# Kernel optimization log

Hardware: AMD Instinct MI355X
Metric: run time of the kernel (lower is better)

The kernel has to match this reference:

```python
import jax, jax.numpy as jnp
import numpy as np
import math

NX = 1024
N_HEAD = 16
HEAD_DIM = NX // N_HEAD
N_CTX = 2048
REL_VOCAB = 64
B = 2
S = 2048


def setup_inputs() -> dict:
    key = jax.random.key(0)
    ks = jax.random.split(key, 7)
    x = jax.random.normal(ks[0], (B, S, NX), dtype=jnp.float32)
    rel = jax.random.randint(ks[1], (B, S, S), 0, REL_VOCAB, dtype=jnp.int64)
    sc = 0.02
    Wqkv = jax.random.normal(ks[2], (NX, 3 * NX), dtype=jnp.float32) * sc
    bqkv = jnp.zeros((3 * NX,), dtype=jnp.float32)
    Wproj = jax.random.normal(ks[3], (NX, NX), dtype=jnp.float32) * sc
    bproj = jnp.zeros((NX,), dtype=jnp.float32)
    rel_emb = jax.random.normal(ks[4], (REL_VOCAB, N_HEAD), dtype=jnp.float32) * sc
    return {"x": x, "Wqkv": Wqkv, "bqkv": bqkv, "Wproj": Wproj,
            "bproj": bproj, "rel_emb": rel_emb, "rel": rel}


def reference(x, Wqkv, bqkv, Wproj, bproj, rel_emb, rel):
    Bsz, Sq, _ = x.shape
    qkv = x @ Wqkv + bqkv                      # [B,S,3*nx]
    q, k, v = jnp.split(qkv, 3, axis=-1)
    def split_heads(t):                        # [B,S,nx] -> [B,H,S,D]
        return t.reshape(Bsz, Sq, N_HEAD, HEAD_DIM).transpose(0, 2, 1, 3)
    q, k, v = split_heads(q), split_heads(k), split_heads(v)
    w = jnp.einsum('bhqd,bhkd->bhqk', q, k) / math.sqrt(HEAD_DIM)
    bmask = jnp.tril(jnp.ones((Sq, Sq), dtype=w.dtype))[None, None]  # [1,1,S,S]
    w = w * bmask - 1e10 * (1.0 - bmask)
    relw = rel_emb[rel].transpose(0, 3, 1, 2)  # [B,S,S,H] -> [B,H,S,S]
    w = w * (relw * bmask)                     # faithful: masked scores become 0
    p = jax.nn.softmax(w, axis=-1)
    a = jnp.einsum('bhqk,bhkd->bhqd', p, v)
    a = a.transpose(0, 2, 1, 3).reshape(Bsz, Sq, NX)  # merge heads
    return a @ Wproj + bproj
```

## Files before the change

### kernel.cpp

```cpp
#include <hip/hip_runtime.h>

typedef unsigned short u16;
typedef unsigned char u8;
typedef __attribute__((ext_vector_type(8))) short short8;
typedef __attribute__((ext_vector_type(4))) short short4v;
typedef __attribute__((ext_vector_type(4))) float f32x4;

#define GLD16(g, l) __builtin_amdgcn_global_load_lds( \
    (const __attribute__((address_space(1))) void*)(g), \
    (__attribute__((address_space(3))) void*)(l), 16, 0, 0)

__device__ __forceinline__ float bf2f(u16 u){
  union { unsigned int i; float f; } v; v.i = ((unsigned int)u) << 16; return v.f;
}
__device__ __forceinline__ u16 f2bf(float f){
  union { float f; unsigned int i; } v; v.f = f;
  unsigned int u = v.i;
  unsigned int r = (u + 0x7FFFu + ((u >> 16) & 1u)) >> 16;
  return (u16)r;
}

__device__ __forceinline__ f32x4 mfma16(short4v a, short4v b, f32x4 c){
#if __has_builtin(__builtin_amdgcn_mfma_f32_16x16x16bf16_1k)
  return __builtin_amdgcn_mfma_f32_16x16x16bf16_1k(a, b, c, 0, 0, 0);
#else
  asm volatile("s_nop 1\n\tv_mfma_f32_16x16x16_bf16 %0, %1, %2, %0" : "+v"(c) : "v"(a), "v"(b));
  return c;
#endif
}

__global__ __launch_bounds__(256) void prep_k(const float* __restrict__ x, u16* __restrict__ xb,
                                              const float* __restrict__ Wqkv, u16* __restrict__ wqkvT,
                                              const float* __restrict__ Wproj, u16* __restrict__ wprojT,
                                              const int* __restrict__ rel, u8* __restrict__ rel8){
  const int bid = blockIdx.x, t = threadIdx.x;
  if (bid < 4096){
    int i = bid * 256 + t;
    float4 v = ((const float4*)x)[i];
    unsigned long long pk = (unsigned long long)f2bf(v.x)
      | ((unsigned long long)f2bf(v.y) << 16)
      | ((unsigned long long)f2bf(v.z) << 32)
      | ((unsigned long long)f2bf(v.w) << 48);
    ((unsigned long long*)xb)[i] = pk;
  } else if (bid < 8192){
    const float* W; u16* Wt; int K, N, blk, nbx;
    if (bid < 7168){ W = Wqkv; Wt = wqkvT; K = 1024; N = 3072; blk = bid - 4096; nbx = 96; }
    else           { W = Wproj; Wt = wprojT; K = 1024; N = 1024; blk = bid - 7168; nbx = 32; }
    __shared__ float tl[32][33];
    int n0 = (blk % nbx) * 32, k0 = (blk / nbx) * 32;
    int tx = t & 31, ty = t >> 5;
    for (int i = ty; i < 32; i += 8)
      tl[i][tx] = W[(size_t)(k0 + i) * N + n0 + tx];
    __syncthreads();
    for (int i = ty; i < 32; i += 8)
      Wt[(size_t)(n0 + i) * K + k0 + tx] = f2bf(tl[tx][i]);
  } else {
    int i = (bid - 8192) * 256 + t;
    int4 v = ((const int4*)rel)[i];
    unsigned int pk = (unsigned int)(v.x & 255) | ((unsigned int)(v.y & 255) << 8)
      | ((unsigned int)(v.z & 255) << 16) | ((unsigned int)(v.w & 255) << 24);
    ((unsigned int*)rel8)[i] = pk;
  }
}

__global__ __launch_bounds__(256) void gemm_qkv_k(const u16* __restrict__ A, const u16* __restrict__ Bt,
                                                  const float* __restrict__ bias,
                                                  u16* __restrict__ oq, u16* __restrict__ okk, u16* __restrict__ vt){
  __shared__ u16 la[3][128 * 32];
  __shared__ u16 lb[3][128 * 32];
  const int K = 1024;
  const int t = threadIdx.x, w = t >> 6, lane = t & 63;
  const int l15 = lane & 15, l4 = lane >> 4;
  const int m0 = blockIdx.y * 128, n0 = blockIdx.x * 128;
  const int wr = w >> 1, wc = w & 1;
  f32x4 acc[4][4] = {};
  const u16* Abase = A + (size_t)m0 * K;
  const u16* Bbase = Bt + (size_t)n0 * K;

  const int srow0 = t >> 2, srow1 = 64 + (t >> 2);
  const int cg = t & 3;
  const int sc0 = cg ^ (srow0 & 3), sc1 = cg ^ (srow1 & 3);
  const int wbase0 = (w * 64) * 8, wbase1 = (256 + w * 64) * 8;

#define QSTAGE(kt, buf) do {                                                        \
    GLD16(Abase + (size_t)srow0 * K + (kt) * 32 + sc0 * 8, &la[buf][wbase0]);       \
    GLD16(Abase + (size_t)srow1 * K + (kt) * 32 + sc1 * 8, &la[buf][wbase1]);       \
    GLD16(Bbase + (size_t)srow0 * K + (kt) * 32 + sc0 * 8, &lb[buf][wbase0]);       \
    GLD16(Bbase + (size_t)srow1 * K + (kt) * 32 + sc1 * 8, &lb[buf][wbase1]);       \
  } while (0)

  QSTAGE(0, 0);
  QSTAGE(1, 1);
  for (int ki = 0; ki < 32; ++ki){
    __builtin_amdgcn_sched_barrier(0);
    if (ki < 31) asm volatile("s_waitcnt vmcnt(4)" ::: "memory");
    else         asm volatile("s_waitcnt vmcnt(0)" ::: "memory");
    __builtin_amdgcn_s_barrier();
    __builtin_amdgcn_sched_barrier(0);
    if (ki + 2 < 32) QSTAGE(ki + 2, (ki + 2) % 3);
    const int cb = ki % 3;
    short8 af[4], bfr[4];
#pragma unroll
    for (int mi = 0; mi < 4; ++mi){
      int row = wr * 64 + mi * 16 + l15;
      af[mi] = *(const short8*)&la[cb][row * 32 + ((l4 ^ (row & 3)) * 8)];
    }
#pragma unroll
    for (int ni = 0; ni < 4; ++ni){
      int row = wc * 64 + ni * 16 + l15;
      bfr[ni] = *(const short8*)&lb[cb][row * 32 + ((l4 ^ (row & 3)) * 8)];
    }
    __builtin_amdgcn_s_setprio(1);
#pragma unroll
    for (int mi = 0; mi < 4; ++mi)
#pragma unroll
      for (int ni = 0; ni < 4; ++ni)
        acc[mi][ni] = __builtin_amdgcn_mfma_f32_16x16x32_bf16(af[mi], bfr[ni], acc[mi][ni], 0, 0, 0);
    __builtin_amdgcn_s_setprio(0);
  }
#undef QSTAGE

#pragma unroll
  for (int mi = 0; mi < 4; ++mi){
    const int m_base = m0 + wr * 64 + mi * 16 + l4 * 4;
    const int bsel = m_base >> 11, s0q = m_base & 2047;
#pragma unroll
    for (int ni = 0; ni < 4; ++ni){
      int n = n0 + wc * 64 + ni * 16 + l15;
      float vb = bias[n];
      int tt = n >> 10, rr = n & 1023, head = rr >> 6, dd = rr & 63;
      if (tt == 2){
        int c = s0q >> 6, w6 = s0q & 63;
        int pj0 = (((w6 >> 2) & 3) << 4) | (((w6 >> 4) & 3) << 2);
        u16 o4[4];
#pragma unroll
        for (int r = 0; r < 4; ++r) o4[r] = f2bf(acc[mi][ni][r] + vb);
        *(uint2*)(vt + ((size_t)(bsel * 16 + head) * 64 + dd) * 2048 + c * 64 + pj0) = *(const uint2*)o4;
      } else {
        u16* dst = (tt == 0) ? oq : okk;
#pragma unroll
        for (int r = 0; r < 4; ++r)
          dst[(((size_t)(bsel * 16 + head)) * 2048 + s0q + r) * 64 + dd] = f2bf(acc[mi][ni][r] + vb);
      }
    }
  }
}

template<int BN>
__global__ __launch_bounds__(256) void gemm_bt_k(const u16* __restrict__ A, const u16* __restrict__ Bt,
                                                 const float* __restrict__ bias, float* __restrict__ of,
                                                 int M, int N, int K){
  __shared__ u16 la[128 * 64];
  __shared__ u16 lb[BN * 64];
  const int t = threadIdx.x, w = t >> 6, lane = t & 63;
  const int l15 = lane & 15, l4 = lane >> 4;
  const int m0 = blockIdx.y * 128, n0 = blockIdx.x * BN;
  const int wr = w >> 1, wc = w & 1;
  constexpr int NI = BN / 32;
  f32x4 acc[4][NI] = {};
  const u16* Abase = A + (size_t)m0 * K;
  const u16* Bbase = Bt + (size_t)n0 * K;
  for (int kt = 0; kt < K; kt += 64){
    __syncthreads();
#pragma unroll
    for (int i = 0; i < 4; ++i){
      int chunk = i * 256 + t;
      int row = chunk >> 3, cs = chunk & 7;
      int c = cs ^ (row & 7);
      GLD16(Abase + (size_t)row * K + kt + c * 8, &la[(i * 256 + w * 64) * 8]);
    }
#pragma unroll
    for (int i = 0; i < BN / 32; ++i){
      int chunk = i * 256 + t;
      int row = chunk >> 3, cs = chunk & 7;
      int c = cs ^ (row & 7);
      GLD16(Bbase + (size_t)row * K + kt + c * 8, &lb[(i * 256 + w * 64) * 8]);
    }
    asm volatile("s_waitcnt vmcnt(0)" ::: "memory");
    __syncthreads();
    short8 af[4][2], bfr[NI][2];
#pragma unroll
    for (int mi = 0; mi < 4; ++mi){
      int row = wr * 64 + mi * 16 + l15;
#pragma unroll
      for (int h = 0; h < 2; ++h)
        af[mi][h] = *(const short8*)&la[row * 64 + (((h * 4 + l4) ^ (row & 7)) * 8)];
    }
#pragma unroll
    for (int ni = 0; ni < NI; ++ni){
      int row = wc * (BN / 2) + ni * 16 + l15;
#pragma unroll
      for (int h = 0; h < 2; ++h)
        bfr[ni][h] = *(const short8*)&lb[row * 64 + (((h * 4 + l4) ^ (row & 7)) * 8)];
    }
#pragma unroll
    for (int mi = 0; mi < 4; ++mi)
#pragma unroll
      for (int ni = 0; ni < NI; ++ni){
        acc[mi][ni] = __builtin_amdgcn_mfma_f32_16x16x32_bf16(af[mi][0], bfr[ni][0], acc[mi][ni], 0, 0, 0);
        acc[mi][ni] = __builtin_amdgcn_mfma_f32_16x16x32_bf16(af[mi][1], bfr[ni][1], acc[mi][ni], 0, 0, 0);
      }
  }
#pragma unroll
  for (int mi = 0; mi < 4; ++mi){
#pragma unroll
    for (int ni = 0; ni < NI; ++ni){
#pragma unroll
      for (int r = 0; r < 4; ++r){
        int m = m0 + wr * 64 + mi * 16 + l4 * 4 + r;
        int n = n0 + wc * (BN / 2) + ni * 16 + l15;
        of[(size_t)m * N + n] = acc[mi][ni][r] + bias[n];
      }
    }
  }
}

__global__ __launch_bounds__(256) void vsuf2_k(const u16* __restrict__ vt, float* __restrict__ vsuf){
  __shared__ float part[32][64];
  const int bh = blockIdx.x;
  const int d = threadIdx.x & 63, qtr = threadIdx.x >> 6;
  const u16* row = vt + ((size_t)bh * 64 + d) * 2048;
  for (int c = qtr * 8; c < qtr * 8 + 8; ++c){
    float s = 0.f;
#pragma unroll
    for (int jv = 0; jv < 8; ++jv){
      short8 v = *(const short8*)(row + c * 64 + jv * 8);
#pragma unroll
      for (int e = 0; e < 8; ++e) s += bf2f((u16)v[e]);
    }
    part[c][d] = s;
  }
  __syncthreads();
  if (threadIdx.x < 64){
    float run = 0.f;
    vsuf[((size_t)bh * 33 + 32) * 64 + d] = 0.f;
    for (int c = 31; c >= 0; --c){
      run += part[c][d];
      vsuf[((size_t)bh * 33 + c) * 64 + d] = run;
    }
  }
}

template<int U8, int SPLIT>
__global__ __launch_bounds__(256, 4) void attn_k(const u16* __restrict__ qb, const u16* __restrict__ kb,
                                                 const u16* __restrict__ vt, const float* __restrict__ vsuf,
                                                 const void* __restrict__ relp, const float* __restrict__ rel_emb,
                                                 u16* __restrict__ ab, float* __restrict__ pacc,
                                                 float* __restrict__ prsum){
  __shared__ u16 Kt[2][64 * 64];
  __shared__ u16 Vt[2][64 * 64];
  __shared__ float remb[64];
  int p, hf, bh;
  if (SPLIT){
    const int lid = blockIdx.x;
    const int bhgrp = lid & 7, within = (lid >> 3) & 3, pf = lid >> 5;
    bh = bhgrp * 4 + within;
    p = pf >> 1; hf = pf & 1;
  } else {
    p = blockIdx.x; hf = 0; bh = blockIdx.y;
  }
  const int b = bh >> 4, h = bh & 15;
  const int TA = p, TB = 31 - p;
  const int q0A = TA * 64, q0B = TB * 64;
  const int tid = threadIdx.x, w = tid >> 6, lane = tid & 63;
  const int l15 = lane & 15, l4 = lane >> 4;
  if (tid < 64) remb[tid] = rel_emb[tid * 16 + h] * (0.125f * 1.44269504088896f);
  const u16* kbh = kb + ((size_t)bh * 2048) * 64;
  const u16* vbh = vt + ((size_t)bh * 64) * 2048;
  const u16* qA = qb + (((size_t)bh * 2048) + q0A + w * 16 + l15) * 64 + l4 * 8;
  const u16* qB = qb + (((size_t)bh * 2048) + q0B + w * 16 + l15) * 64 + l4 * 8;
  const short8 aqA0 = *(const short8*)qA, aqA1 = *(const short8*)(qA + 32);
  const short8 aqB0 = *(const short8*)qB, aqB1 = *(const short8*)(qB + 32);
  const u8*  r8A  = (const u8*)relp + ((size_t)b * 2048 + q0A + w * 16 + l15) * 2048;
  const u8*  r8B  = (const u8*)relp + ((size_t)b * 2048 + q0B + w * 16 + l15) * 2048;
  const int* r32A = (const int*)relp + ((size_t)b * 2048 + q0A + w * 16 + l15) * 2048;
  const int* r32B = (const int*)relp + ((size_t)b * 2048 + q0B + w * 16 + l15) * 2048;

  const int srow0 = (tid >> 3), srow1 = 32 + (tid >> 3);
  const int scs = tid & 7;
  const int sc0 = scs ^ (srow0 & 7), sc1 = scs ^ (srow1 & 7);
  const int sldsoff = (w * 64) * 8;

#define STAGE(ktile, buf) do {                                                       \
    GLD16(kbh + (size_t)((ktile) * 64 + srow0) * 64 + sc0 * 8, &Kt[buf][sldsoff]);   \
    GLD16(kbh + (size_t)((ktile) * 64 + srow1) * 64 + sc1 * 8, &Kt[buf][2048 + sldsoff]); \
    GLD16(vbh + (size_t)srow0 * 2048 + (ktile) * 64 + sc0 * 8, &Vt[buf][sldsoff]);   \
    GLD16(vbh + (size_t)srow1 * 2048 + (ktile) * 64 + sc1 * 8, &Vt[buf][2048 + sldsoff]); \
  } while (0)

  f32x4 acc[4] = {};
  float rsum = 0.f;
  unsigned int relc[4], reln[4];

  auto relload = [&](bool isA, int kt, unsigned int* dst){
    int off = kt * 64 + 4 * l4;
    if (U8){
      const u8* pp = isA ? r8A : r8B;
#pragma unroll
      for (int t = 0; t < 4; ++t) dst[t] = *(const unsigned int*)(pp + off + 16 * t);
    } else {
      const int* pp = isA ? r32A : r32B;
#pragma unroll
      for (int t = 0; t < 4; ++t){
        int4 v4 = *(const int4*)(pp + off + 16 * t);
        dst[t] = (unsigned int)(v4.x & 255) | ((unsigned int)(v4.y & 255) << 8)
               | ((unsigned int)(v4.z & 255) << 16) | ((unsigned int)(v4.w & 255) << 24);
      }
    }
  };

  auto writeout = [&](int Td, int q0){
    asm volatile("s_nop 7\n\ts_nop 7" :::);
    float s = rsum;
    s += __shfl_xor(s, 16);
    s += __shfl_xor(s, 32);
    float invZ = 1.f / (s + (float)(2048 - (Td + 1) * 64));
    int qg = q0 + w * 16 + l15;
    const float* sufp = vsuf + ((size_t)bh * 33 + Td + 1) * 64;
#pragma unroll
    for (int ni = 0; ni < 4; ++ni){
      float4 sv = *(const float4*)(sufp + ni * 16 + 4 * l4);
      unsigned int lo2 = (unsigned int)f2bf((acc[ni][0] + sv.x) * invZ)
                       | ((unsigned int)f2bf((acc[ni][1] + sv.y) * invZ) << 16);
      unsigned int hi2 = (unsigned int)f2bf((acc[ni][2] + sv.z) * invZ)
                       | ((unsigned int)f2bf((acc[ni][3] + sv.w) * invZ) << 16);
      uint2 o; o.x = lo2; o.y = hi2;
      *(uint2*)(ab + ((size_t)b * 2048 + qg) * 1024 + h * 64 + ni * 16 + 4 * l4) = o;
    }
  };

  const int lo = (SPLIT && hf) ? 17 : 0;
  const int hi = (SPLIT && !hf) ? 17 : 33;

  {
    bool isA0 = (lo <= TA);
    int kt0 = isA0 ? lo : lo - TA - 1;
    STAGE(kt0, 0);
    relload(isA0, kt0, relc);
  }
  __syncthreads();

  for (int it = lo; it < hi; ++it){
    const bool isA = (it <= TA);
    const int kt = isA ? it : (it - TA - 1);
    const int cur = (it - lo) & 1;

    if (it + 1 < hi){
      const bool nA = (it + 1 <= TA);
      const int nkt = nA ? (it + 1) : (it - TA);
      STAGE(nkt, cur ^ 1);
      relload(nA, nkt, reln);
    }

    const short8 a0 = isA ? aqA0 : aqB0;
    const short8 a1 = isA ? aqA1 : aqB1;
    const bool diag = (kt == (isA ? TA : TB));

    short4v pk[4];
    __builtin_amdgcn_s_setprio(1);
#pragma unroll
    for (int t = 0; t < 4; ++t){
      const int krow = 16 * t + l15;
      const u16* kbase = &Kt[cur][krow * 64];
      short8 bk0 = *(const short8*)&kbase[((l4)     ^ (krow & 7)) * 8];
      short8 bk1 = *(const short8*)&kbase[((4 + l4) ^ (krow & 7)) * 8];
      f32x4 sf = {0.f, 0.f, 0.f, 0.f};
      sf = __builtin_amdgcn_mfma_f32_16x16x32_bf16(bk0, a0, sf, 0, 0, 0);
      sf = __builtin_amdgcn_mfma_f32_16x16x32_bf16(bk1, a1, sf, 0, 0, 0);
      unsigned int rw = relc[t];
      const int kk = 16 * t + 4 * l4;
      float prv[4];
#pragma unroll
      for (int r = 0; r < 4; ++r){
        float sc = sf[r] * remb[(rw >> (8 * r)) & 255];
        if (diag) sc = (kk + r <= w * 16 + l15) ? sc : 0.f;
        float pv = __builtin_amdgcn_exp2f(sc);
        rsum += pv;
        prv[r] = pv;
      }
      union { unsigned int u[2]; short4v s; } pu;
      asm("v_cvt_pk_bf16_f32 %0, %1, %2" : "=v"(pu.u[0]) : "v"(prv[0]), "v"(prv[1]));
      asm("v_cvt_pk_bf16_f32 %0, %1, %2" : "=v"(pu.u[1]) : "v"(prv[2]), "v"(prv[3]));
      pk[t] = pu.s;
    }
    asm volatile("s_nop 2" :::);
#pragma unroll
    for (int ni = 0; ni < 4; ++ni){
      const int drow = ni * 16 + l15;
      const u16* vbase = &Vt[cur][drow * 64];
      short8 vv0 = *(const short8*)&vbase[(((2 * l4)     ^ (drow & 7))) * 8];
      short8 vv1 = *(const short8*)&vbase[(((2 * l4 + 1) ^ (drow & 7))) * 8];
      short4v va0 = {vv0[0], vv0[1], vv0[2], vv0[3]};
      short4v va1 = {vv0[4], vv0[5], vv0[6], vv0[7]};
      short4v va2 = {vv1[0], vv1[1], vv1[2], vv1[3]};
      short4v va3 = {vv1[4], vv1[5], vv1[6], vv1[7]};
      acc[ni] = mfma16(va0, pk[0], acc[ni]);
      acc[ni] = mfma16(va1, pk[1], acc[ni]);
      acc[ni] = mfma16(va2, pk[2], acc[ni]);
      acc[ni] = mfma16(va3, pk[3], acc[ni]);
    }
    __builtin_amdgcn_s_setprio(0);

    if (it == TA){
      writeout(TA, q0A);
#pragma unroll
      for (int ni = 0; ni < 4; ++ni) acc[ni] = f32x4{0.f, 0.f, 0.f, 0.f};
      rsum = 0.f;
    }
    if (it + 1 < hi){
#pragma unroll
      for (int t = 0; t < 4; ++t) relc[t] = reln[t];
    }
    __syncthreads();
  }
#undef STAGE

  if (SPLIT){
    asm volatile("s_nop 7\n\ts_nop 7" :::);
    float s = rsum;
    s += __shfl_xor(s, 16);
    s += __shfl_xor(s, 32);
    const size_t slot = (((size_t)bh * 16 + p) * 2 + hf);
    float* pslot = pacc + slot * 4096;
#pragma unroll
    for (int ni = 0; ni < 4; ++ni)
      *(f32x4*)(pslot + (w * 16 + l15) * 64 + ni * 16 + 4 * l4) = acc[ni];
    if (l4 == 0) prsum[slot * 64 + w * 16 + l15] = s;
  } else {
    writeout(TB, q0B);
  }
}

__global__ __launch_bounds__(256) void attn_fin_k(const float* __restrict__ pacc,
                                                  const float* __restrict__ prsum,
                                                  const float* __restrict__ vsuf,
                                                  u16* __restrict__ ab){
  const int p = blockIdx.x, bh = blockIdx.y;
  const int b = bh >> 4, h = bh & 15;
  const int TB = 31 - p, q0 = TB * 64;
  const int r = threadIdx.x >> 2, cg = threadIdx.x & 3;
  const size_t slot = ((size_t)bh * 16 + p) * 2;
  const size_t base = slot * 4096 + r * 64 + cg * 16;
  float rs = prsum[slot * 64 + r] + prsum[(slot + 1) * 64 + r];
  float invZ = 1.f / (rs + (float)(2048 - (TB + 1) * 64));
  const float* sufp = vsuf + ((size_t)bh * 33 + TB + 1) * 64 + cg * 16;
  u16 o[16];
#pragma unroll
  for (int j = 0; j < 4; ++j){
    f32x4 a0 = *(const f32x4*)(pacc + base + j * 4);
    f32x4 a1 = *(const f32x4*)(pacc + base + 4096 + j * 4);
    f32x4 sv = *(const f32x4*)(sufp + j * 4);
#pragma unroll
    for (int e = 0; e < 4; ++e) o[j * 4 + e] = f2bf((a0[e] + a1[e] + sv[e]) * invZ);
  }
  u16* dst = ab + ((size_t)b * 2048 + q0 + r) * 1024 + h * 64 + cg * 16;
  *(uint4*)dst = *(const uint4*)&o[0];
  *(uint4*)(dst + 8) = *(const uint4*)&o[8];
}

extern "C" void kernel_launch(void* const* d_in, const int* in_sizes, int n_in,
                              void* d_out, int out_size, void* d_ws, size_t ws_size,
                              hipStream_t stream){
  const float* x       = (const float*)d_in[0];
  const float* Wqkv    = (const float*)d_in[1];
  const float* bqkv    = (const float*)d_in[2];
  const float* Wproj   = (const float*)d_in[3];
  const float* bproj   = (const float*)d_in[4];
  const float* rel_emb = (const float*)d_in[5];
  const int*   rel     = (const int*)d_in[6];
  float* out = (float*)d_out;

  char* ws = (char*)d_ws;
  u16* xb     = (u16*)(ws);
  u16* wqkvT  = (u16*)(ws + (8ull  << 20));
  u16* wprojT = (u16*)(ws + (14ull << 20));
  u16* qb     = (u16*)(ws + (16ull << 20));
  u16* kb     = (u16*)(ws + (24ull << 20));
  u16* vtb    = (u16*)(ws + (40ull << 20));
  float* vsuf = (float*)(ws + (48ull << 20));
  float* pacc = (float*)(ws + (49ull << 20));
  float* prsum= (float*)(ws + (65ull << 20) + (512ull << 10));
  u8*   rel8  = (u8*)(ws + (66ull << 20));
  const bool useSplit = ws_size >= (67ull << 20);
  const bool useU8    = ws_size >= (75ull << 20);

  prep_k<<<useU8 ? 16384 : 8192, 256, 0, stream>>>(x, xb, Wqkv, wqkvT, Wproj, wprojT, rel, rel8);
  gemm_qkv_k<<<dim3(24, 32), 256, 0, stream>>>(xb, wqkvT, bqkv, qb, kb, vtb);
  vsuf2_k<<<32, 256, 0, stream>>>(vtb, vsuf);
  if (useU8)
    attn_k<1, 1><<<dim3(1024), 256, 0, stream>>>(qb, kb, vtb, vsuf, rel8, rel_emb, xb, pacc, prsum);
  else if (useSplit)
    attn_k<0, 1><<<dim3(1024), 256, 0, stream>>>(qb, kb, vtb, vsuf, rel, rel_emb, xb, pacc, prsum);
  else
    attn_k<0, 0><<<dim3(16, 32), 256, 0, stream>>>(qb, kb, vtb, vsuf, rel, rel_emb, xb, pacc, prsum);
  if (useSplit || useU8)
    attn_fin_k<<<dim3(16, 32), 256, 0, stream>>>(pacc, prsum, vsuf, xb);
  gemm_bt_k<64><<<dim3(16, 32), 256, 0, stream>>>(xb, wprojT, bproj, out, 4096, 1024, 1024);
}
```

Measured before the change: 138.9 us.

## Triple-buffer projection GEMM loads and replace LDS rel-emb lookup with bpermute

```diff
diff --git a/kernel.cpp b/kernel.cpp
--- a/kernel.cpp
+++ b/kernel.cpp
@@ -146,69 +146,69 @@
   }
 }
 
-template<int BN>
-__global__ __launch_bounds__(256) void gemm_bt_k(const u16* __restrict__ A, const u16* __restrict__ Bt,
-                                                 const float* __restrict__ bias, float* __restrict__ of,
-                                                 int M, int N, int K){
-  __shared__ u16 la[128 * 64];
-  __shared__ u16 lb[BN * 64];
+__global__ __launch_bounds__(256) void gemm_proj_k(const u16* __restrict__ A, const u16* __restrict__ Bt,
+                                                   const float* __restrict__ bias, float* __restrict__ of){
+  __shared__ u16 la[3][128 * 32];
+  __shared__ u16 lb[3][64 * 32];
+  const int K = 1024, N = 1024;
   const int t = threadIdx.x, w = t >> 6, lane = t & 63;
   const int l15 = lane & 15, l4 = lane >> 4;
-  const int m0 = blockIdx.y * 128, n0 = blockIdx.x * BN;
+  const int m0 = blockIdx.y * 128, n0 = blockIdx.x * 64;
   const int wr = w >> 1, wc = w & 1;
-  constexpr int NI = BN / 32;
-  f32x4 acc[4][NI] = {};
+  f32x4 acc[4][2] = {};
   const u16* Abase = A + (size_t)m0 * K;
   const u16* Bbase = Bt + (size_t)n0 * K;
-  for (int kt = 0; kt < K; kt += 64){
-    __syncthreads();
-#pragma unroll
-    for (int i = 0; i < 4; ++i){
-      int chunk = i * 256 + t;
-      int row = chunk >> 3, cs = chunk & 7;
-      int c = cs ^ (row & 7);
-      GLD16(Abase + (size_t)row * K + kt + c * 8, &la[(i * 256 + w * 64) * 8]);
-    }
-#pragma unroll
-    for (int i = 0; i < BN / 32; ++i){
-      int chunk = i * 256 + t;
-      int row = chunk >> 3, cs = chunk & 7;
-      int c = cs ^ (row & 7);
-      GLD16(Bbase + (size_t)row * K + kt + c * 8, &lb[(i * 256 + w * 64) * 8]);
-    }
-    asm volatile("s_waitcnt vmcnt(0)" ::: "memory");
-    __syncthreads();
-    short8 af[4][2], bfr[NI][2];
+
+  const int srow0 = t >> 2, srow1 = 64 + (t >> 2);
+  const int cg = t & 3;
+  const int sc0 = cg ^ (srow0 & 3), sc1 = cg ^ (srow1 & 3);
+  const int wbase0 = (w * 64) * 8, wbase1 = (256 + w * 64) * 8;
+
+#define PSTAGE(kt, buf) do {                                                        \
+    GLD16(Abase + (size_t)srow0 * K + (kt) * 32 + sc0 * 8, &la[buf][wbase0]);       \
+    GLD16(Abase + (size_t)srow1 * K + (kt) * 32 + sc1 * 8, &la[buf][wbase1]);       \
+    GLD16(Bbase + (size_t)srow0 * K + (kt) * 32 + sc0 * 8, &lb[buf][wbase0]);       \
+  } while (0)
+
+  PSTAGE(0, 0);
+  PSTAGE(1, 1);
+  for (int ki = 0; ki < 32; ++ki){
+    __builtin_amdgcn_sched_barrier(0);
+    if (ki < 31) asm volatile("s_waitcnt vmcnt(3)" ::: "memory");
+    else         asm volatile("s_waitcnt vmcnt(0)" ::: "memory");
+    __builtin_amdgcn_s_barrier();
+    __builtin_amdgcn_sched_barrier(0);
+    if (ki + 2 < 32) PSTAGE(ki + 2, (ki + 2) % 3);
+    const int cb = ki % 3;
+    short8 af[4], bfr[2];
 #pragma unroll
     for (int mi = 0; mi < 4; ++mi){
       int row = wr * 64 + mi * 16 + l15;
-#pragma unroll
-      for (int h = 0; h < 2; ++h)
-        af[mi][h] = *(const short8*)&la[row * 64 + (((h * 4 + l4) ^ (row & 7)) * 8)];
-    }
-#pragma unroll
-    for (int ni = 0; ni < NI; ++ni){
-      int row = wc * (BN / 2) + ni * 16 + l15;
-#pragma unroll
-      for (int h = 0; h < 2; ++h)
-        bfr[ni][h] = *(const short8*)&lb[row * 64 + (((h * 4 + l4) ^ (row & 7)) * 8)];
-    }
+      af[mi] = *(const short8*)&la[cb][row * 32 + ((l4 ^ (row & 3)) * 8)];
+    }
+#pragma unroll
+    for (int ni = 0; ni < 2; ++ni){
+      int row = wc * 32 + ni * 16 + l15;
+      bfr[ni] = *(const short8*)&lb[cb][row * 32 + ((l4 ^ (row & 3)) * 8)];
+    }
+    __builtin_amdgcn_s_setprio(1);
 #pragma unroll
     for (int mi = 0; mi < 4; ++mi)
 #pragma unroll
-      for (int ni = 0; ni < NI; ++ni){
-        acc[mi][ni] = __builtin_amdgcn_mfma_f32_16x16x32_bf16(af[mi][0], bfr[ni][0], acc[mi][ni], 0, 0, 0);
-        acc[mi][ni] = __builtin_amdgcn_mfma_f32_16x16x32_bf16(af[mi][1], bfr[ni][1], acc[mi][ni], 0, 0, 0);
-      }
-  }
+      for (int ni = 0; ni < 2; ++ni)
+        acc[mi][ni] = __builtin_amdgcn_mfma_f32_16x16x32_bf16(af[mi], bfr[ni], acc[mi][ni], 0, 0, 0);
+    __builtin_amdgcn_s_setprio(0);
+  }
+#undef PSTAGE
+
 #pragma unroll
   for (int mi = 0; mi < 4; ++mi){
 #pragma unroll
-    for (int ni = 0; ni < NI; ++ni){
+    for (int ni = 0; ni < 2; ++ni){
 #pragma unroll
       for (int r = 0; r < 4; ++r){
         int m = m0 + wr * 64 + mi * 16 + l4 * 4 + r;
-        int n = n0 + wc * (BN / 2) + ni * 16 + l15;
+        int n = n0 + wc * 32 + ni * 16 + l15;
         of[(size_t)m * N + n] = acc[mi][ni][r] + bias[n];
       }
     }
@@ -249,7 +249,6 @@
                                                  float* __restrict__ prsum){
   __shared__ u16 Kt[2][64 * 64];
   __shared__ u16 Vt[2][64 * 64];
-  __shared__ float remb[64];
   int p, hf, bh;
   if (SPLIT){
     const int lid = blockIdx.x;
@@ -264,7 +263,7 @@
   const int q0A = TA * 64, q0B = TB * 64;
   const int tid = threadIdx.x, w = tid >> 6, lane = tid & 63;
   const int l15 = lane & 15, l4 = lane >> 4;
-  if (tid < 64) remb[tid] = rel_emb[tid * 16 + h] * (0.125f * 1.44269504088896f);
+  const int remb_bits = __float_as_int(rel_emb[lane * 16 + h] * (0.125f * 1.44269504088896f));
   const u16* kbh = kb + ((size_t)bh * 2048) * 64;
   const u16* vbh = vt + ((size_t)bh * 64) * 2048;
   const u16* qA = qb + (((size_t)bh * 2048) + q0A + w * 16 + l15) * 64 + l4 * 8;
@@ -372,7 +371,9 @@
       float prv[4];
 #pragma unroll
       for (int r = 0; r < 4; ++r){
-        float sc = sf[r] * remb[(rw >> (8 * r)) & 255];
+        int idx4 = (int)((rw >> (8 * r)) & 255u) << 2;
+        float rwf = __int_as_float(__builtin_amdgcn_ds_bpermute(idx4, remb_bits));
+        float sc = sf[r] * rwf;
         if (diag) sc = (kk + r <= w * 16 + l15) ? sc : 0.f;
         float pv = __builtin_amdgcn_exp2f(sc);
         rsum += pv;
@@ -495,5 +496,5 @@
     attn_k<0, 0><<<dim3(16, 32), 256, 0, stream>>>(qb, kb, vtb, vsuf, rel, rel_emb, xb, pacc, prsum);
   if (useSplit || useU8)
     attn_fin_k<<<dim3(16, 32), 256, 0, stream>>>(pacc, prsum, vsuf, xb);
-  gemm_bt_k<64><<<dim3(16, 32), 256, 0, stream>>>(xb, wprojT, bproj, out, 4096, 1024, 1024);
-}
+  gemm_proj_k<<<dim3(16, 32), 256, 0, stream>>>(xb, wprojT, bproj, out);
+}
```

After: 142.0 us. 2.3% more time.

## Split attention key range into three chunks with bf16 partials and bpermute lookup

Applied to the files above, without the earlier changes.

```diff
diff --git a/kernel.cpp b/kernel.cpp
--- a/kernel.cpp
+++ b/kernel.cpp
@@ -245,26 +245,25 @@
 __global__ __launch_bounds__(256, 4) void attn_k(const u16* __restrict__ qb, const u16* __restrict__ kb,
                                                  const u16* __restrict__ vt, const float* __restrict__ vsuf,
                                                  const void* __restrict__ relp, const float* __restrict__ rel_emb,
-                                                 u16* __restrict__ ab, float* __restrict__ pacc,
+                                                 u16* __restrict__ ab, u16* __restrict__ paccb,
                                                  float* __restrict__ prsum){
   __shared__ u16 Kt[2][64 * 64];
   __shared__ u16 Vt[2][64 * 64];
-  __shared__ float remb[64];
-  int p, hf, bh;
+  int p, u_, bh;
   if (SPLIT){
     const int lid = blockIdx.x;
-    const int bhgrp = lid & 7, within = (lid >> 3) & 3, pf = lid >> 5;
+    const int bhgrp = lid & 7, within = (lid >> 3) & 3, pu = lid >> 5;
     bh = bhgrp * 4 + within;
-    p = pf >> 1; hf = pf & 1;
+    p = pu / 3; u_ = pu % 3;
   } else {
-    p = blockIdx.x; hf = 0; bh = blockIdx.y;
+    p = blockIdx.x; u_ = 0; bh = blockIdx.y;
   }
   const int b = bh >> 4, h = bh & 15;
   const int TA = p, TB = 31 - p;
   const int q0A = TA * 64, q0B = TB * 64;
   const int tid = threadIdx.x, w = tid >> 6, lane = tid & 63;
   const int l15 = lane & 15, l4 = lane >> 4;
-  if (tid < 64) remb[tid] = rel_emb[tid * 16 + h] * (0.125f * 1.44269504088896f);
+  const int remb_bits = __float_as_int(rel_emb[lane * 16 + h] * (0.125f * 1.44269504088896f));
   const u16* kbh = kb + ((size_t)bh * 2048) * 64;
   const u16* vbh = vt + ((size_t)bh * 64) * 2048;
   const u16* qA = qb + (((size_t)bh * 2048) + q0A + w * 16 + l15) * 64 + l4 * 8;
@@ -329,8 +328,26 @@
     }
   };
 
-  const int lo = (SPLIT && hf) ? 17 : 0;
-  const int hi = (SPLIT && !hf) ? 17 : 33;
+  auto emitP = [&](int t01){
+    asm volatile("s_nop 7\n\ts_nop 7" :::);
+    float s = rsum;
+    s += __shfl_xor(s, 16);
+    s += __shfl_xor(s, 32);
+    const size_t slot = (((size_t)bh * 16 + p) * 3 + u_) * 2 + t01;
+    u16* pbase = paccb + slot * 4096 + (size_t)(w * 16 + l15) * 64;
+#pragma unroll
+    for (int ni = 0; ni < 4; ++ni){
+      unsigned int w0, w1;
+      asm("v_cvt_pk_bf16_f32 %0, %1, %2" : "=v"(w0) : "v"(acc[ni][0]), "v"(acc[ni][1]));
+      asm("v_cvt_pk_bf16_f32 %0, %1, %2" : "=v"(w1) : "v"(acc[ni][2]), "v"(acc[ni][3]));
+      uint2 o; o.x = w0; o.y = w1;
+      *(uint2*)(pbase + ni * 16 + 4 * l4) = o;
+    }
+    if (l4 == 0) prsum[slot * 64 + w * 16 + l15] = s;
+  };
+
+  const int lo = SPLIT ? 11 * u_ : 0;
+  const int hi = SPLIT ? lo + 11 : 33;
 
   {
     bool isA0 = (lo <= TA);
@@ -372,16 +389,18 @@
       float prv[4];
 #pragma unroll
       for (int r = 0; r < 4; ++r){
-        float sc = sf[r] * remb[(rw >> (8 * r)) & 255];
+        int idx4 = (int)((rw >> (8 * r)) & 255u) << 2;
+        float rwf = __int_as_float(__builtin_amdgcn_ds_bpermute(idx4, remb_bits));
+        float sc = sf[r] * rwf;
         if (diag) sc = (kk + r <= w * 16 + l15) ? sc : 0.f;
         float pv = __builtin_amdgcn_exp2f(sc);
         rsum += pv;
         prv[r] = pv;
       }
-      union { unsigned int u[2]; short4v s; } pu;
-      asm("v_cvt_pk_bf16_f32 %0, %1, %2" : "=v"(pu.u[0]) : "v"(prv[0]), "v"(prv[1]));
-      asm("v_cvt_pk_bf16_f32 %0, %1, %2" : "=v"(pu.u[1]) : "v"(prv[2]), "v"(prv[3]));
-      pk[t] = pu.s;
+      union { unsigned int u[2]; short4v s; } pu2;
+      asm("v_cvt_pk_bf16_f32 %0, %1, %2" : "=v"(pu2.u[0]) : "v"(prv[0]), "v"(prv[1]));
+      asm("v_cvt_pk_bf16_f32 %0, %1, %2" : "=v"(pu2.u[1]) : "v"(prv[2]), "v"(prv[3]));
+      pk[t] = pu2.s;
     }
     asm volatile("s_nop 2" :::);
 #pragma unroll
@@ -402,7 +421,8 @@
     __builtin_amdgcn_s_setprio(0);
 
     if (it == TA){
-      writeout(TA, q0A);
+      if (SPLIT) emitP(0);
+      else       writeout(TA, q0A);
 #pragma unroll
       for (int ni = 0; ni < 4; ++ni) acc[ni] = f32x4{0.f, 0.f, 0.f, 0.f};
       rsum = 0.f;
@@ -416,44 +436,46 @@
 #undef STAGE
 
   if (SPLIT){
-    asm volatile("s_nop 7\n\ts_nop 7" :::);
-    float s = rsum;
-    s += __shfl_xor(s, 16);
-    s += __shfl_xor(s, 32);
-    const size_t slot = (((size_t)bh * 16 + p) * 2 + hf);
-    float* pslot = pacc + slot * 4096;
-#pragma unroll
-    for (int ni = 0; ni < 4; ++ni)
-      *(f32x4*)(pslot + (w * 16 + l15) * 64 + ni * 16 + 4 * l4) = acc[ni];
-    if (l4 == 0) prsum[slot * 64 + w * 16 + l15] = s;
+    if (TA >= hi)           emitP(0);
+    else if (TA != hi - 1)  emitP(1);
   } else {
     writeout(TB, q0B);
   }
 }
 
-__global__ __launch_bounds__(256) void attn_fin_k(const float* __restrict__ pacc,
-                                                  const float* __restrict__ prsum,
-                                                  const float* __restrict__ vsuf,
-                                                  u16* __restrict__ ab){
-  const int p = blockIdx.x, bh = blockIdx.y;
+__global__ __launch_bounds__(256) void attn_fin2_k(const u16* __restrict__ pa,
+                                                   const float* __restrict__ pr,
+                                                   const float* __restrict__ vsuf,
+                                                   u16* __restrict__ ab){
+  const int qt = blockIdx.x, bh = blockIdx.y;
   const int b = bh >> 4, h = bh & 15;
-  const int TB = 31 - p, q0 = TB * 64;
+  const bool isB = qt >= 16;
+  const int p = isB ? 31 - qt : qt;
+  const int u0 = isB ? (p + 1) / 11 : 0;
+  const int u1 = isB ? 3 : (p / 11 + 1);
+  const int t01 = isB ? 1 : 0;
   const int r = threadIdx.x >> 2, cg = threadIdx.x & 3;
-  const size_t slot = ((size_t)bh * 16 + p) * 2;
-  const size_t base = slot * 4096 + r * 64 + cg * 16;
-  float rs = prsum[slot * 64 + r] + prsum[(slot + 1) * 64 + r];
-  float invZ = 1.f / (rs + (float)(2048 - (TB + 1) * 64));
-  const float* sufp = vsuf + ((size_t)bh * 33 + TB + 1) * 64 + cg * 16;
+  float av[16] = {};
+  float rs = 0.f;
+  for (int uu = u0; uu < u1; ++uu){
+    const size_t slot = (((size_t)bh * 16 + p) * 3 + uu) * 2 + t01;
+    const u16* sp = pa + slot * 4096 + (size_t)r * 64 + cg * 16;
+    uint4 w0 = *(const uint4*)sp;
+    uint4 w1 = *(const uint4*)(sp + 8);
+    const u16* pw0 = (const u16*)&w0;
+    const u16* pw1 = (const u16*)&w1;
+#pragma unroll
+    for (int j = 0; j < 8; ++j) av[j] += bf2f(pw0[j]);
+#pragma unroll
+    for (int j = 0; j < 8; ++j) av[8 + j] += bf2f(pw1[j]);
+    rs += pr[slot * 64 + r];
+  }
+  float invZ = 1.f / (rs + (float)(2048 - (qt + 1) * 64));
+  const float* sufp = vsuf + ((size_t)bh * 33 + qt + 1) * 64 + cg * 16;
   u16 o[16];
 #pragma unroll
-  for (int j = 0; j < 4; ++j){
-    f32x4 a0 = *(const f32x4*)(pacc + base + j * 4);
-    f32x4 a1 = *(const f32x4*)(pacc + base + 4096 + j * 4);
-    f32x4 sv = *(const f32x4*)(sufp + j * 4);
-#pragma unroll
-    for (int e = 0; e < 4; ++e) o[j * 4 + e] = f2bf((a0[e] + a1[e] + sv[e]) * invZ);
-  }
-  u16* dst = ab + ((size_t)b * 2048 + q0 + r) * 1024 + h * 64 + cg * 16;
+  for (int j = 0; j < 16; ++j) o[j] = f2bf((av[j] + sufp[j]) * invZ);
+  u16* dst = ab + ((size_t)b * 2048 + qt * 64 + r) * 1024 + h * 64 + cg * 16;
   *(uint4*)dst = *(const uint4*)&o[0];
   *(uint4*)(dst + 8) = *(const uint4*)&o[8];
 }
@@ -476,24 +498,24 @@
   u16* wprojT = (u16*)(ws + (14ull << 20));
   u16* qb     = (u16*)(ws + (16ull << 20));
   u16* kb     = (u16*)(ws + (24ull << 20));
+  u8*   rel8  = (u8*)(ws + (32ull << 20));
   u16* vtb    = (u16*)(ws + (40ull << 20));
   float* vsuf = (float*)(ws + (48ull << 20));
-  float* pacc = (float*)(ws + (49ull << 20));
-  float* prsum= (float*)(ws + (65ull << 20) + (512ull << 10));
-  u8*   rel8  = (u8*)(ws + (66ull << 20));
-  const bool useSplit = ws_size >= (67ull << 20);
-  const bool useU8    = ws_size >= (75ull << 20);
+  u16* paccb  = (u16*)(ws + (49ull << 20));
+  float* prsum= (float*)(ws + (73ull << 20));
+  const bool useSplit = ws_size >= (74ull << 20);
+  const bool useU8    = ws_size >= (41ull << 20);
 
   prep_k<<<useU8 ? 16384 : 8192, 256, 0, stream>>>(x, xb, Wqkv, wqkvT, Wproj, wprojT, rel, rel8);
   gemm_qkv_k<<<dim3(24, 32), 256, 0, stream>>>(xb, wqkvT, bqkv, qb, kb, vtb);
   vsuf2_k<<<32, 256, 0, stream>>>(vtb, vsuf);
-  if (useU8)
-    attn_k<1, 1><<<dim3(1024), 256, 0, stream>>>(qb, kb, vtb, vsuf, rel8, rel_emb, xb, pacc, prsum);
-  else if (useSplit)
-    attn_k<0, 1><<<dim3(1024), 256, 0, stream>>>(qb, kb, vtb, vsuf, rel, rel_emb, xb, pacc, prsum);
-  else
-    attn_k<0, 0><<<dim3(16, 32), 256, 0, stream>>>(qb, kb, vtb, vsuf, rel, rel_emb, xb, pacc, prsum);
-  if (useSplit || useU8)
-    attn_fin_k<<<dim3(16, 32), 256, 0, stream>>>(pacc, prsum, vsuf, xb);
+  if (useSplit && useU8){
+    attn_k<1, 1><<<dim3(1536), 256, 0, stream>>>(qb, kb, vtb, vsuf, rel8, rel_emb, xb, paccb, prsum);
+    attn_fin2_k<<<dim3(32, 32), 256, 0, stream>>>(paccb, prsum, vsuf, xb);
+  } else if (useU8){
+    attn_k<1, 0><<<dim3(16, 32), 256, 0, stream>>>(qb, kb, vtb, vsuf, rel8, rel_emb, xb, paccb, prsum);
+  } else {
+    attn_k<0, 0><<<dim3(16, 32), 256, 0, stream>>>(qb, kb, vtb, vsuf, rel, rel_emb, xb, paccb, prsum);
+  }
   gemm_bt_k<64><<<dim3(16, 32), 256, 0, stream>>>(xb, wprojT, bproj, out, 4096, 1024, 1024);
 }
```

Measured after the change: 141.3 us. About the same (+1.7%).
